# Optimization experiments

Hardware: AMD Instinct MI355X
Metric: run time of the kernel (lower is better)

Reference implementation:

```python
import jax, jax.numpy as jnp
import numpy as np

N_NODES = 50000
N_EDGES = 800000
D = 128


def setup_inputs() -> dict:
    key = jax.random.key(0)
    k1, k2, k3, k4, k5 = jax.random.split(key, 5)
    node_attr = jax.random.normal(k1, (N_NODES, D), dtype=jnp.float32)
    edge_index = jax.random.randint(k2, (2, N_EDGES), 0, N_NODES, dtype=jnp.int64)
    edge_attr = jax.random.normal(k3, (N_EDGES, D), dtype=jnp.float32)
    # 2-layer MLP: (3D -> D) -> ReLU -> (D -> D), scaled init
    w1 = jax.random.normal(k4, (3 * D, D), dtype=jnp.float32) * (1.0 / np.sqrt(3 * D))
    b1 = jnp.zeros((D,), dtype=jnp.float32)
    w2 = jax.random.normal(k5, (D, D), dtype=jnp.float32) * (1.0 / np.sqrt(D))
    b2 = jnp.zeros((D,), dtype=jnp.float32)
    return {"node_attr": node_attr, "edge_index": edge_index, "edge_attr": edge_attr,
            "w1": w1, "b1": b1, "w2": w2, "b2": b2}


def reference(node_attr, edge_index, edge_attr, w1, b1, w2, b2):
    senders_idx = edge_index[0]
    receivers_idx = edge_index[1]
    senders_attr = node_attr[senders_idx]      # [E, D] irregular gather
    receivers_attr = node_attr[receivers_idx]  # [E, D] irregular gather
    collected = jnp.concatenate([senders_attr, receivers_attr, edge_attr], axis=1)  # [E, 3D]
    h = jax.nn.relu(collected @ w1 + b1)       # [E, D]
    edge_attr_new = h @ w2 + b2                # [E, D]
    return edge_attr_new
```

## Files before the change

### kernel.cpp

```cpp
#include <hip/hip_runtime.h>


#define NE 800000
#define ND 50000
#define DD 128

typedef float f32x4v __attribute__((ext_vector_type(4)));
typedef float f32x16 __attribute__((ext_vector_type(16)));
typedef _Float16 f16x8 __attribute__((ext_vector_type(8)));
typedef _Float16 f16x4 __attribute__((ext_vector_type(4)));

__device__ __forceinline__ f16x4 cvt4(f32x4v v) {
    f16x4 r;
    r[0] = (_Float16)v[0]; r[1] = (_Float16)v[1];
    r[2] = (_Float16)v[2]; r[3] = (_Float16)v[3];
    return r;
}

__global__ void prep_w(const float* __restrict__ w1, const float* __restrict__ w2,
                       _Float16* __restrict__ w1t, _Float16* __restrict__ w2f) {
    int i = blockIdx.x * 256 + threadIdx.x;
    if (i < 384 * 128) {
        int col = i / 384;
        int k = i - col * 384;
        float v = w1[(size_t)k * 128 + col];
        int byteoff = col * 768 + ((k * 2) ^ ((col & 15) << 4));
        *(_Float16*)((char*)w1t + byteoff) = (_Float16)v;
    } else {
        int j = i - 384 * 128;
        int kk2 = j >> 10;
        int col = (j >> 3) & 127;
        int jj = j & 7;
        w2f[j] = (_Float16)w2[(size_t)(kk2 * 8 + jj) * 128 + col];
    }
}

__global__ void prep_node(const float* __restrict__ node_attr, _Float16* __restrict__ nf16) {
    int i = blockIdx.x * 256 + threadIdx.x;
    const float* src = node_attr + (size_t)i * 8;
    f32x4v a = *(const f32x4v*)src;
    f32x4v b = *(const f32x4v*)(src + 4);
    f16x8 r;
    r[0] = (_Float16)a[0]; r[1] = (_Float16)a[1];
    r[2] = (_Float16)a[2]; r[3] = (_Float16)a[3];
    r[4] = (_Float16)b[0]; r[5] = (_Float16)b[1];
    r[6] = (_Float16)b[2]; r[7] = (_Float16)b[3];
    *(f16x8*)(nf16 + (size_t)i * 8) = r;
}

#define MFMA_SEG(SEG)                                                                     \
    _Pragma("unroll")                                                                     \
    for (int kk8 = 0; kk8 < 8; kk8++) {                                                   \
        f16x8 a = *(const f16x8*)(ab + r31 * 256 + ((kk8 * 32 + g2 * 16) ^ xa));          \
        _Pragma("unroll")                                                                 \
        for (int n = 0; n < 4; n++) {                                                     \
            const int col = n * 32 + r31;                                                 \
            f16x8 b = *(const f16x8*)(lds + col * 768 +                                   \
                       ((((SEG) * 8 + kk8) * 32 + g2 * 16) ^ ((col & 15) << 4)));         \
            acc[n] = __builtin_amdgcn_mfma_f32_32x32x16_f16(a, b, acc[n], 0, 0, 0);       \
        }                                                                                 \
    }

#define WRITE_SEG16(V)                                                                    \
    _Pragma("unroll")                                                                     \
    for (int i = 0; i < 16; i++) {                                                        \
        const int row = 2 * i + g2;                                                       \
        *(f16x4*)(ab + row * 256 + ((r31 * 8) ^ ((row & 15) << 4))) = V[i];               \
    }

__global__ __attribute__((amdgpu_flat_work_group_size(512, 512),
                          amdgpu_waves_per_eu(2, 2)))
void edge_mlp(
    const float* __restrict__ node_attr,
    const int* __restrict__ eidx,
    const float* __restrict__ edge_attr,
    const _Float16* __restrict__ w1t,
    const float* __restrict__ b1,
    const _Float16* __restrict__ w2f,
    const float* __restrict__ b2,
    const _Float16* __restrict__ nf16,
    float* __restrict__ out) {
    extern __shared__ char lds[];

    const int tid = threadIdx.x;
    const int wid = tid >> 6;
    const int lane = tid & 63;
    const int r31 = lane & 31;
    const int g2 = lane >> 5;

    const int ebase = blockIdx.x * 256 + wid * 32;

    const int sidx = eidx[ebase + r31];
    const int ridx = eidx[NE + ebase + r31];

    {
        const char* src = (const char*)w1t;
        #pragma unroll
        for (int i = 0; i < 12; i++) {
            int off = (tid + i * 512) * 16;
            *(f16x8*)(lds + off) = *(const f16x8*)(src + off);
        }
    }

    float b1v[4], b2v[4];
    #pragma unroll
    for (int n = 0; n < 4; n++) { b1v[n] = b1[n * 32 + r31]; b2v[n] = b2[n * 32 + r31]; }

    __syncthreads();

    char* ab = lds + 96 * 1024 + wid * 8192;
    const int xa = (r31 & 15) << 4;

    f32x4v ev[16];
    #pragma unroll
    for (int i = 0; i < 16; i++) {
        const int row = 2 * i + g2;
        ev[i] = __builtin_nontemporal_load(
            (const f32x4v*)(edge_attr + (size_t)(ebase + row) * DD + r31 * 4));
    }
    f16x4 sv[16];
    #pragma unroll
    for (int i = 0; i < 16; i++) {
        int r = __shfl(sidx, 2 * i + g2);
        sv[i] = *(const f16x4*)(nf16 + (size_t)r * DD + r31 * 4);
    }
    __builtin_amdgcn_sched_barrier(0);

    #pragma unroll
    for (int i = 0; i < 16; i++) {
        const int row = 2 * i + g2;
        *(f16x4*)(ab + row * 256 + ((r31 * 8) ^ ((row & 15) << 4))) = cvt4(ev[i]);
    }

    f16x4 rv[16];
    #pragma unroll
    for (int i = 0; i < 16; i++) {
        int r = __shfl(ridx, 2 * i + g2);
        rv[i] = *(const f16x4*)(nf16 + (size_t)r * DD + r31 * 4);
    }

    f32x16 acc[4] = {};
    __builtin_amdgcn_wave_barrier();

    MFMA_SEG(2)

    WRITE_SEG16(sv)
    __builtin_amdgcn_wave_barrier();

    MFMA_SEG(0)

    WRITE_SEG16(rv)
    f16x8 b2fa[4][4];
    #pragma unroll
    for (int kk = 0; kk < 4; kk++)
        #pragma unroll
        for (int n = 0; n < 4; n++)
            b2fa[kk][n] = *(const f16x8*)(w2f + ((size_t)((kk * 2 + g2) * 128 + n * 32 + r31)) * 8);
    __builtin_amdgcn_wave_barrier();

    MFMA_SEG(1)

    #pragma unroll
    for (int n = 0; n < 4; n++) {
        const int col = n * 32 + r31;
        #pragma unroll
        for (int reg = 0; reg < 16; reg++) {
            const int row = (reg & 3) + 8 * (reg >> 2) + 4 * g2;
            float v = fmaxf(acc[n][reg] + b1v[n], 0.0f);
            *(_Float16*)(ab + row * 256 + ((col * 2) ^ ((row & 15) << 4))) = (_Float16)v;
        }
    }
    __builtin_amdgcn_wave_barrier();

    f32x16 acc2[4] = {};
    #pragma unroll
    for (int kk = 0; kk < 4; kk++) {
        f16x8 a = *(const f16x8*)(ab + r31 * 256 + ((kk * 32 + g2 * 16) ^ xa));
        #pragma unroll
        for (int n = 0; n < 4; n++)
            acc2[n] = __builtin_amdgcn_mfma_f32_32x32x16_f16(a, b2fa[kk][n], acc2[n], 0, 0, 0);
    }
    f16x8 b2fb[4][4];
    #pragma unroll
    for (int kk = 0; kk < 4; kk++)
        #pragma unroll
        for (int n = 0; n < 4; n++)
            b2fb[kk][n] = *(const f16x8*)(w2f + ((size_t)(((kk + 4) * 2 + g2) * 128 + n * 32 + r31)) * 8);
    #pragma unroll
    for (int kk = 4; kk < 8; kk++) {
        f16x8 a = *(const f16x8*)(ab + r31 * 256 + ((kk * 32 + g2 * 16) ^ xa));
        #pragma unroll
        for (int n = 0; n < 4; n++)
            acc2[n] = __builtin_amdgcn_mfma_f32_32x32x16_f16(a, b2fb[kk - 4][n], acc2[n], 0, 0, 0);
    }

    #pragma unroll
    for (int n = 0; n < 4; n++) {
        #pragma unroll
        for (int reg = 0; reg < 16; reg++) {
            const int row = (reg & 3) + 8 * (reg >> 2) + 4 * g2;
            __builtin_nontemporal_store(acc2[n][reg] + b2v[n],
                out + (size_t)(ebase + row) * DD + n * 32 + r31);
        }
    }
}

extern "C" void kernel_launch(void* const* d_in, const int* in_sizes, int n_in,
                              void* d_out, int out_size, void* d_ws, size_t ws_size,
                              hipStream_t stream) {
    const float* node_attr = (const float*)d_in[0];
    const int* eidx = (const int*)d_in[1];
    const float* edge_attr = (const float*)d_in[2];
    const float* w1 = (const float*)d_in[3];
    const float* b1 = (const float*)d_in[4];
    const float* w2 = (const float*)d_in[5];
    const float* b2 = (const float*)d_in[6];
    float* out = (float*)d_out;

    _Float16* w1t = (_Float16*)d_ws;
    _Float16* w2f = w1t + 384 * 128;
    _Float16* nf16 = w2f + 128 * 128;

    hipFuncSetAttribute((const void*)edge_mlp,
                        hipFuncAttributeMaxDynamicSharedMemorySize, 160 * 1024);

    prep_w<<<256, 256, 0, stream>>>(w1, w2, w1t, w2f);
    prep_node<<<3125, 256, 0, stream>>>(node_attr, nf16);
    edge_mlp<<<3125, 512, 160 * 1024, stream>>>(node_attr, eidx, edge_attr,
                                                w1t, b1, w2f, b2, nf16, out);
}
```

Baseline: 253.0 us.

## Switch to 16x16x32 MFMA with 16-edge waves and 1024-thread blocks

Each wave now processes 16 edges instead of 32, using 16x16x32 f16 MFMA tiles in place of 32x32x16, and the block grows to 16 waves (1024 threads) with half the per-wave LDS staging. The gather and segment order is also changed: the sender and receiver node rows are staged first and the edge_attr load is deferred and overlapped with the MFMA segments. The goal is more waves in flight to hide the latency of the irregular gathers. The cost is more LDS B-fragment reads per MFMA, because the weights are reused over only 16 rows per wave.

```diff
diff --git a/kernel.cpp b/kernel.cpp
--- a/kernel.cpp
+++ b/kernel.cpp
@@ -6,7 +6,6 @@
 #define DD 128
 
 typedef float f32x4v __attribute__((ext_vector_type(4)));
-typedef float f32x16 __attribute__((ext_vector_type(16)));
 typedef _Float16 f16x8 __attribute__((ext_vector_type(8)));
 typedef _Float16 f16x4 __attribute__((ext_vector_type(4)));
 
@@ -28,10 +27,10 @@
         *(_Float16*)((char*)w1t + byteoff) = (_Float16)v;
     } else {
         int j = i - 384 * 128;
-        int kk2 = j >> 10;
+        int ks = j >> 10;
         int col = (j >> 3) & 127;
         int jj = j & 7;
-        w2f[j] = (_Float16)w2[(size_t)(kk2 * 8 + jj) * 128 + col];
+        w2f[j] = (_Float16)w2[(size_t)(ks * 8 + jj) * 128 + col];
     }
 }
 
@@ -50,26 +49,26 @@
 
 #define MFMA_SEG(SEG)                                                                     \
     _Pragma("unroll")                                                                     \
-    for (int kk8 = 0; kk8 < 8; kk8++) {                                                   \
-        f16x8 a = *(const f16x8*)(ab + r31 * 256 + ((kk8 * 32 + g2 * 16) ^ xa));          \
+    for (int kk = 0; kk < 4; kk++) {                                                      \
+        f16x8 a = *(const f16x8*)(ab + r15 * 256 + ((kk * 64 + q16) ^ xa));               \
         _Pragma("unroll")                                                                 \
-        for (int n = 0; n < 4; n++) {                                                     \
-            const int col = n * 32 + r31;                                                 \
+        for (int n = 0; n < 8; n++) {                                                     \
+            const int col = n * 16 + r15;                                                 \
             f16x8 b = *(const f16x8*)(lds + col * 768 +                                   \
-                       ((((SEG) * 8 + kk8) * 32 + g2 * 16) ^ ((col & 15) << 4)));         \
-            acc[n] = __builtin_amdgcn_mfma_f32_32x32x16_f16(a, b, acc[n], 0, 0, 0);       \
+                       ((((SEG) * 4 + kk) * 64 + q16) ^ xa));                             \
+            acc[n] = __builtin_amdgcn_mfma_f32_16x16x32_f16(a, b, acc[n], 0, 0, 0);       \
         }                                                                                 \
     }
 
 #define WRITE_SEG16(V)                                                                    \
     _Pragma("unroll")                                                                     \
-    for (int i = 0; i < 16; i++) {                                                        \
-        const int row = 2 * i + g2;                                                       \
-        *(f16x4*)(ab + row * 256 + ((r31 * 8) ^ ((row & 15) << 4))) = V[i];               \
-    }
-
-__global__ __attribute__((amdgpu_flat_work_group_size(512, 512),
-                          amdgpu_waves_per_eu(2, 2)))
+    for (int i = 0; i < 8; i++) {                                                         \
+        const int row = 2 * i + sub;                                                      \
+        *(f16x4*)(ab + row * 256 + ((c31 * 8) ^ ((row & 15) << 4))) = V[i];               \
+    }
+
+__global__ __attribute__((amdgpu_flat_work_group_size(1024, 1024),
+                          amdgpu_waves_per_eu(4, 4)))
 void edge_mlp(
     const float* __restrict__ node_attr,
     const int* __restrict__ eidx,
@@ -85,122 +84,126 @@
     const int tid = threadIdx.x;
     const int wid = tid >> 6;
     const int lane = tid & 63;
-    const int r31 = lane & 31;
-    const int g2 = lane >> 5;
-
-    const int ebase = blockIdx.x * 256 + wid * 32;
-
-    const int sidx = eidx[ebase + r31];
-    const int ridx = eidx[NE + ebase + r31];
+    const int r15 = lane & 15;
+    const int q16 = (lane >> 4) * 16;
+    const int sub = lane >> 5;
+    const int c31 = lane & 31;
 
     {
         const char* src = (const char*)w1t;
         #pragma unroll
-        for (int i = 0; i < 12; i++) {
-            int off = (tid + i * 512) * 16;
+        for (int i = 0; i < 6; i++) {
+            int off = (tid + i * 1024) * 16;
             *(f16x8*)(lds + off) = *(const f16x8*)(src + off);
         }
     }
 
-    float b1v[4], b2v[4];
-    #pragma unroll
-    for (int n = 0; n < 4; n++) { b1v[n] = b1[n * 32 + r31]; b2v[n] = b2[n * 32 + r31]; }
+    float b1v[8], b2v[8];
+    #pragma unroll
+    for (int n = 0; n < 8; n++) { b1v[n] = b1[n * 16 + r15]; b2v[n] = b2[n * 16 + r15]; }
 
     __syncthreads();
 
-    char* ab = lds + 96 * 1024 + wid * 8192;
-    const int xa = (r31 & 15) << 4;
-
-    f32x4v ev[16];
-    #pragma unroll
-    for (int i = 0; i < 16; i++) {
-        const int row = 2 * i + g2;
+    char* ab = lds + 96 * 1024 + wid * 4096;
+    const int xa = r15 << 4;
+    const int ebase = blockIdx.x * 256 + wid * 16;
+
+    const int sidx = eidx[ebase + r15];
+    const int ridx = eidx[NE + ebase + r15];
+
+    f16x4 sv[8];
+    #pragma unroll
+    for (int i = 0; i < 8; i++) {
+        int r = __shfl(sidx, 2 * i + sub);
+        sv[i] = *(const f16x4*)(nf16 + (size_t)r * DD + c31 * 4);
+    }
+    WRITE_SEG16(sv)
+
+    f16x4 rv[8];
+    #pragma unroll
+    for (int i = 0; i < 8; i++) {
+        int r = __shfl(ridx, 2 * i + sub);
+        rv[i] = *(const f16x4*)(nf16 + (size_t)r * DD + c31 * 4);
+    }
+
+    typedef float f32x4a __attribute__((ext_vector_type(4)));
+    f32x4a acc[8] = {};
+    __builtin_amdgcn_wave_barrier();
+
+    MFMA_SEG(0)
+
+    WRITE_SEG16(rv)
+    f32x4v ev[8];
+    #pragma unroll
+    for (int i = 0; i < 8; i++) {
+        const int row = 2 * i + sub;
         ev[i] = __builtin_nontemporal_load(
-            (const f32x4v*)(edge_attr + (size_t)(ebase + row) * DD + r31 * 4));
-    }
-    f16x4 sv[16];
-    #pragma unroll
-    for (int i = 0; i < 16; i++) {
-        int r = __shfl(sidx, 2 * i + g2);
-        sv[i] = *(const f16x4*)(nf16 + (size_t)r * DD + r31 * 4);
-    }
-    __builtin_amdgcn_sched_barrier(0);
-
-    #pragma unroll
-    for (int i = 0; i < 16; i++) {
-        const int row = 2 * i + g2;
-        *(f16x4*)(ab + row * 256 + ((r31 * 8) ^ ((row & 15) << 4))) = cvt4(ev[i]);
-    }
-
-    f16x4 rv[16];
-    #pragma unroll
-    for (int i = 0; i < 16; i++) {
-        int r = __shfl(ridx, 2 * i + g2);
-        rv[i] = *(const f16x4*)(nf16 + (size_t)r * DD + r31 * 4);
-    }
-
-    f32x16 acc[4] = {};
+            (const f32x4v*)(edge_attr + (size_t)(ebase + row) * DD + c31 * 4));
+    }
+    __builtin_amdgcn_wave_barrier();
+
+    MFMA_SEG(1)
+
+    #pragma unroll
+    for (int i = 0; i < 8; i++) {
+        const int row = 2 * i + sub;
+        *(f16x4*)(ab + row * 256 + ((c31 * 8) ^ ((row & 15) << 4))) = cvt4(ev[i]);
+    }
+    f16x8 b2fa[2][8];
+    #pragma unroll
+    for (int kk = 0; kk < 2; kk++)
+        #pragma unroll
+        for (int n = 0; n < 8; n++) {
+            const int ks = kk * 4 + (lane >> 4);
+            b2fa[kk][n] = *(const f16x8*)(w2f + ((size_t)(ks * 128 + n * 16 + r15)) * 8);
+        }
     __builtin_amdgcn_wave_barrier();
 
     MFMA_SEG(2)
 
-    WRITE_SEG16(sv)
-    __builtin_amdgcn_wave_barrier();
-
-    MFMA_SEG(0)
-
-    WRITE_SEG16(rv)
-    f16x8 b2fa[4][4];
-    #pragma unroll
-    for (int kk = 0; kk < 4; kk++)
-        #pragma unroll
-        for (int n = 0; n < 4; n++)
-            b2fa[kk][n] = *(const f16x8*)(w2f + ((size_t)((kk * 2 + g2) * 128 + n * 32 + r31)) * 8);
-    __builtin_amdgcn_wave_barrier();
-
-    MFMA_SEG(1)
-
-    #pragma unroll
-    for (int n = 0; n < 4; n++) {
-        const int col = n * 32 + r31;
-        #pragma unroll
-        for (int reg = 0; reg < 16; reg++) {
-            const int row = (reg & 3) + 8 * (reg >> 2) + 4 * g2;
+    #pragma unroll
+    for (int n = 0; n < 8; n++) {
+        const int col = n * 16 + r15;
+        #pragma unroll
+        for (int reg = 0; reg < 4; reg++) {
+            const int row = (lane >> 4) * 4 + reg;
             float v = fmaxf(acc[n][reg] + b1v[n], 0.0f);
             *(_Float16*)(ab + row * 256 + ((col * 2) ^ ((row & 15) << 4))) = (_Float16)v;
         }
     }
     __builtin_amdgcn_wave_barrier();
 
-    f32x16 acc2[4] = {};
-    #pragma unroll
-    for (int kk = 0; kk < 4; kk++) {
-        f16x8 a = *(const f16x8*)(ab + r31 * 256 + ((kk * 32 + g2 * 16) ^ xa));
-        #pragma unroll
-        for (int n = 0; n < 4; n++)
-            acc2[n] = __builtin_amdgcn_mfma_f32_32x32x16_f16(a, b2fa[kk][n], acc2[n], 0, 0, 0);
-    }
-    f16x8 b2fb[4][4];
-    #pragma unroll
-    for (int kk = 0; kk < 4; kk++)
-        #pragma unroll
-        for (int n = 0; n < 4; n++)
-            b2fb[kk][n] = *(const f16x8*)(w2f + ((size_t)(((kk + 4) * 2 + g2) * 128 + n * 32 + r31)) * 8);
-    #pragma unroll
-    for (int kk = 4; kk < 8; kk++) {
-        f16x8 a = *(const f16x8*)(ab + r31 * 256 + ((kk * 32 + g2 * 16) ^ xa));
-        #pragma unroll
-        for (int n = 0; n < 4; n++)
-            acc2[n] = __builtin_amdgcn_mfma_f32_32x32x16_f16(a, b2fb[kk - 4][n], acc2[n], 0, 0, 0);
-    }
-
-    #pragma unroll
-    for (int n = 0; n < 4; n++) {
-        #pragma unroll
-        for (int reg = 0; reg < 16; reg++) {
-            const int row = (reg & 3) + 8 * (reg >> 2) + 4 * g2;
+    f32x4a acc2[8] = {};
+    #pragma unroll
+    for (int kk = 0; kk < 2; kk++) {
+        f16x8 a = *(const f16x8*)(ab + r15 * 256 + ((kk * 64 + q16) ^ xa));
+        #pragma unroll
+        for (int n = 0; n < 8; n++)
+            acc2[n] = __builtin_amdgcn_mfma_f32_16x16x32_f16(a, b2fa[kk][n], acc2[n], 0, 0, 0);
+    }
+    f16x8 b2fb[2][8];
+    #pragma unroll
+    for (int kk = 0; kk < 2; kk++)
+        #pragma unroll
+        for (int n = 0; n < 8; n++) {
+            const int ks = (kk + 2) * 4 + (lane >> 4);
+            b2fb[kk][n] = *(const f16x8*)(w2f + ((size_t)(ks * 128 + n * 16 + r15)) * 8);
+        }
+    #pragma unroll
+    for (int kk = 2; kk < 4; kk++) {
+        f16x8 a = *(const f16x8*)(ab + r15 * 256 + ((kk * 64 + q16) ^ xa));
+        #pragma unroll
+        for (int n = 0; n < 8; n++)
+            acc2[n] = __builtin_amdgcn_mfma_f32_16x16x32_f16(a, b2fb[kk - 2][n], acc2[n], 0, 0, 0);
+    }
+
+    #pragma unroll
+    for (int n = 0; n < 8; n++) {
+        #pragma unroll
+        for (int reg = 0; reg < 4; reg++) {
+            const int row = (lane >> 4) * 4 + reg;
             __builtin_nontemporal_store(acc2[n][reg] + b2v[n],
-                out + (size_t)(ebase + row) * DD + n * 32 + r31);
+                out + (size_t)(ebase + row) * DD + n * 16 + r15);
         }
     }
 }
@@ -226,6 +229,6 @@
 
     prep_w<<<256, 256, 0, stream>>>(w1, w2, w1t, w2f);
     prep_node<<<3125, 256, 0, stream>>>(node_attr, nf16);
-    edge_mlp<<<3125, 512, 160 * 1024, stream>>>(node_attr, eidx, edge_attr,
-                                                w1t, b1, w2f, b2, nf16, out);
-}
+    edge_mlp<<<3125, 1024, 160 * 1024, stream>>>(node_attr, eidx, edge_attr,
+                                                 w1t, b1, w2f, b2, nf16, out);
+}
```

Result: slower. 377.8 us (+49.3%).
